# Kernel tuning notes

Measured on AMD Instinct MI355X. Metric: run time of the kernel, lower is better.

## Reference

```python
import jax, jax.numpy as jnp
import numpy as np

B, N, DM, S = 128, 1024, 64, 2
D_IN = 1 + 1 + 2 + DM  # x(1) + m(1) + u(2) + h(DM)


def setup_inputs() -> dict:
    key = jax.random.key(0)
    ks = jax.random.split(key, 12)
    return {
        "x": jax.random.normal(ks[0], (B, 1, N), jnp.float32),
        "m": jax.random.uniform(ks[1], (B, 1, N), jnp.float32),
        "u": jax.random.normal(ks[2], (B, 2, N), jnp.float32),
        "h": jax.random.normal(ks[3], (B, DM, N), jnp.float32),
        # stack of support_len row-normalized-ish adjacencies [S, N, N]
        "adj": jax.random.uniform(ks[4], (S, N, N), jnp.float32) / N,
        "W_in": jax.random.normal(ks[5], (DM, D_IN), jnp.float32) * 0.05,
        "b_in": jnp.zeros((DM,), jnp.float32),
        "W_gc": jax.random.normal(ks[6], (DM, S * DM), jnp.float32) * 0.05,
        "b_gc": jnp.zeros((DM,), jnp.float32),
        "W_out": jax.random.normal(ks[7], (DM, 2 * DM), jnp.float32) * 0.05,
        "b_out": jnp.zeros((DM,), jnp.float32),
        "W_read": jax.random.normal(ks[8], (1, 2 * DM), jnp.float32) * 0.05,
        "b_read": jnp.zeros((1,), jnp.float32),
        "prelu_w": jnp.full((1,), 0.25, jnp.float32),
    }


def _conv1x1(x, W, b):
    # Conv1d(kernel_size=1): [b,c,n] x [o,c] -> [b,o,n]
    return jnp.einsum('bcn,oc->bon', x, W) + b[None, :, None]


def reference(x, m, u, h, adj, W_in, b_in, W_gc, b_gc, W_out, b_out, W_read, b_read, prelu_w):
    # concat inputs on channel dim, then 1x1 conv to d_model
    x_in = jnp.concatenate([x, m, u, h], axis=1)            # [b, d_in, n]
    x_in = _conv1x1(x_in, W_in, b_in)                        # [b, dm, n]
    # SpatialConvOrderK (order=1, include_self=False):
    # per-support aggregation einsum('ncvl,wv->ncwl') with l==1
    agg = jnp.einsum('bcv,swv->bscw', x_in, adj)             # [b, S, dm, n]
    b_, s_, c_, n_ = agg.shape
    agg = agg.reshape(b_, s_ * c_, n_)                       # support-major concat
    gc = _conv1x1(agg, W_gc, b_gc)                           # [b, dm, n]
    out = jnp.concatenate([gc, h], axis=1)                   # [b, 2dm, n]
    out = _conv1x1(out, W_out, b_out)
    out = jnp.where(out >= 0, out, prelu_w[0] * out)         # PReLU (1 param)
    out = jnp.concatenate([out, h], axis=1)                  # [b, 2dm, n]
    return _conv1x1(out, W_read, b_read), out
```

## Files before the change

kernel.cpp:

```cpp
#include <hip/hip_runtime.h>
#include <hip/hip_bf16.h>
#include <stdint.h>

#define NB 128
#define NN 1024
#define NDM 64

typedef __bf16 bf16;
typedef __bf16 bf16x8_t __attribute__((ext_vector_type(8)));
typedef __bf16 bf16x4_t __attribute__((ext_vector_type(4)));
typedef float f32x4 __attribute__((ext_vector_type(4)));

__global__ __launch_bounds__(256) void k_prep(
    const float* __restrict__ adj,
    const float* __restrict__ W_in, const float* __restrict__ b_in,
    const float* __restrict__ W_gc, const float* __restrict__ b_gc,
    const float* __restrict__ W_out, const float* __restrict__ b_out,
    const float* __restrict__ W_read,
    bf16* __restrict__ adjb, bf16* __restrict__ WAT, float* __restrict__ WYX,
    float* __restrict__ BIAS, bf16* __restrict__ W1B, bf16* __restrict__ A2B,
    float* __restrict__ HBv) {
  const int bx = blockIdx.x;
  if (bx < 2048) {
    int i = bx * 256 + threadIdx.x;
    float4 v = reinterpret_cast<const float4*>(adj)[i];
    bf16x4_t r;
    r.x = (bf16)v.x; r.y = (bf16)v.y; r.z = (bf16)v.z; r.w = (bf16)v.w;
    reinterpret_cast<bf16x4_t*>(adjb)[i] = r;
    return;
  }
  int i = (bx - 2048) * 256 + threadIdx.x;
  if (i < 8192) {
    int r = i >> 6, cc = i & 63;
    int cq = cc >> 3, j = cc & 7;
    int c = ((cq ^ (r & 7)) << 3) + j;
    int s = r >> 6, o = r & 63;
    float val = 0.f;
    for (int k = 0; k < 64; ++k) val += W_gc[o * 128 + s * 64 + k] * W_in[k * 68 + 4 + c];
    WAT[i] = (bf16)val;
  } else if (i < 8704) {
    int idx = i - 8192;
    int r = idx >> 2, jj = idx & 3;
    int s = r >> 6, o = r & 63;
    float val = 0.f;
    for (int k = 0; k < 64; ++k) val += W_gc[o * 128 + s * 64 + k] * W_in[k * 68 + jj];
    WYX[idx] = val;
  } else if (i < 8832) {
    int r = i - 8704;
    int s = r >> 6, o = r & 63;
    float val = 0.f;
    for (int k = 0; k < 64; ++k) val += W_gc[o * 128 + s * 64 + k] * b_in[k];
    BIAS[r] = val;
  } else if (i < 12928) {
    int j = i - 8832;
    int o = j >> 6, c = j & 63;
    W1B[j] = (bf16)W_out[o * 128 + c];
  } else if (i < 18048) {
    int j = i - 12928;
    int r = j >> 6, c = j & 63;
    float val = 0.f;
    if (r < 64) val = W_out[r * 128 + 64 + c];
    else if (r == 64) val = W_read[64 + c];
    A2B[j] = (bf16)val;
  } else if (i < 18112) {
    int o = i - 18048;
    float val = b_out[o];
    for (int c = 0; c < 64; ++c) val += W_out[o * 128 + c] * b_gc[c];
    HBv[o] = val;
  }
}

__global__ __launch_bounds__(256) void k_build(
    const float* __restrict__ x, const float* __restrict__ m, const float* __restrict__ u,
    const float* __restrict__ h, const bf16* __restrict__ WAT,
    const float* __restrict__ WYX, const float* __restrict__ BIAS,
    bf16* __restrict__ Y, bf16* __restrict__ HT, float* __restrict__ out2) {
  __shared__ __align__(16) float T[64 * 128];
  __shared__ __align__(16) bf16 HTs[128 * 64];
  __shared__ __align__(16) bf16 WAs[128 * 64];
  __shared__ __align__(16) float X4L[128 * 4];
  __shared__ __align__(16) float WYXs[128 * 4];
  __shared__ __align__(16) float biasL[128];
  const int t = threadIdx.x;
  const int vb = blockIdx.x * 128;
  const int b = blockIdx.y;

  for (int i = t; i < 2048; i += 256)
    __builtin_amdgcn_global_load_lds(
        (const uint32_t*)(h + (size_t)(b * 64 + (i >> 5)) * NN + vb + (i & 31) * 4),
        (uint32_t*)&T[i * 4], 16, 0, 0);
  for (int i = t; i < 1024; i += 256)
    __builtin_amdgcn_global_load_lds((const uint32_t*)(WAT + i * 8), (uint32_t*)&WAs[i * 8], 16, 0, 0);
  if (t < 128)
    __builtin_amdgcn_global_load_lds((const uint32_t*)(WYX + t * 4), (uint32_t*)&WYXs[t * 4], 16, 0, 0);
  if (t < 32)
    __builtin_amdgcn_global_load_lds((const uint32_t*)(BIAS + t * 4), (uint32_t*)&biasL[t * 4], 16, 0, 0);
  if (t < 128) {
    float4 x4;
    x4.x = x[(size_t)b * NN + vb + t];
    x4.y = m[(size_t)b * NN + vb + t];
    x4.z = u[(size_t)(b * 2) * NN + vb + t];
    x4.w = u[(size_t)(b * 2 + 1) * NN + vb + t];
    *reinterpret_cast<float4*>(&X4L[t * 4]) = x4;
  }
  __syncthreads();

  {
    const int v = t >> 1, half = t & 1;
#pragma unroll
    for (int cc = 0; cc < 4; ++cc) {
      int cq = half * 4 + cc;
      int cbase = (cq ^ (v & 7)) << 3;
      bf16x8_t pk;
#pragma unroll
      for (int j = 0; j < 8; ++j) pk[j] = (bf16)T[(cbase + j) * 128 + v];
      *reinterpret_cast<bf16x8_t*>(&HTs[v * 64 + cq * 8]) = pk;
      *reinterpret_cast<bf16x8_t*>(&HT[((size_t)(b << 10) + vb + v) * 64 + cq * 8]) = pk;
    }
  }
  for (int i = t; i < 2048; i += 256) {
    int r = i >> 5, ck = i & 31;
    float4 hv = *reinterpret_cast<const float4*>(&T[r * 128 + ck * 4]);
    *reinterpret_cast<float4*>(&out2[(size_t)(b * 128 + 64 + r) * NN + vb + ck * 4]) = hv;
  }
  __syncthreads();

  const int wave = t >> 6, lane = t & 63;
  const int q = lane >> 4, lx = lane & 7, o16 = lane & 15;
  const int offK0 = (q ^ lx) << 3, offK1 = ((q + 4) ^ lx) << 3;

#pragma unroll
  for (int vi = 0; vi < 2; ++vi) {
    const int vt = wave + vi * 4;
    const int vrow = vt * 16 + o16;
    bf16x8_t af0 = *reinterpret_cast<const bf16x8_t*>(&HTs[vrow * 64 + offK0]);
    bf16x8_t af1 = *reinterpret_cast<const bf16x8_t*>(&HTs[vrow * 64 + offK1]);
    float4 x4r[4];
#pragma unroll
    for (int r = 0; r < 4; ++r)
      x4r[r] = *reinterpret_cast<const float4*>(&X4L[(vt * 16 + q * 4 + r) * 4]);
    const int vg = vb + vt * 16 + q * 4;
    for (int nt = 0; nt < 8; ++nt) {
      const int rr = nt * 16 + o16;
      bf16x8_t bf0 = *reinterpret_cast<const bf16x8_t*>(&WAs[rr * 64 + offK0]);
      bf16x8_t bf1 = *reinterpret_cast<const bf16x8_t*>(&WAs[rr * 64 + offK1]);
      float bsv = biasL[rr];
      float4 wy = *reinterpret_cast<const float4*>(&WYXs[rr * 4]);
      f32x4 c0;
#pragma unroll
      for (int r = 0; r < 4; ++r)
        c0[r] = bsv + wy.x * x4r[r].x + wy.y * x4r[r].y + wy.z * x4r[r].z + wy.w * x4r[r].w;
      f32x4 acc = __builtin_amdgcn_mfma_f32_16x16x32_bf16(af0, bf0, c0, 0, 0, 0);
      acc = __builtin_amdgcn_mfma_f32_16x16x32_bf16(af1, bf1, acc, 0, 0, 0);
      const int s = nt >> 2;
      const int o = rr - s * 64;
      bf16x4_t pk;
      pk.x = (bf16)acc[0]; pk.y = (bf16)acc[1]; pk.z = (bf16)acc[2]; pk.w = (bf16)acc[3];
      *reinterpret_cast<bf16x4_t*>(&Y[(size_t)(b * 64 + o) * 2048 + s * 1024 + vg]) = pk;
    }
  }
}

__global__ __launch_bounds__(256) void k_gemm(
    const bf16* __restrict__ Y, const bf16* __restrict__ ADJB,
    const bf16* __restrict__ HT,
    const bf16* __restrict__ W1B, const bf16* __restrict__ A2B,
    const float* __restrict__ HBv, const float* __restrict__ W_read,
    const float* __restrict__ b_read, const float* __restrict__ prelu_w,
    float* __restrict__ out0, float* __restrict__ out2) {
  __shared__ __align__(16) union SMem {
    struct { bf16 As[128 * 64]; bf16 Bs[128 * 64]; } st;
    bf16 gcs[2 * 128 * 72];
  } sm;
  __shared__ __align__(16) bf16 W1s[64 * 72];
  __shared__ __align__(16) bf16 A2s[80 * 72];
  __shared__ float HBs[64];
  __shared__ float Wrs[64];

  const int t = threadIdx.x;
  const int wave = t >> 6, lane = t & 63;
  const int rowA = blockIdx.x * 128;
  const int colB = blockIdx.y * 128;
  const int wm = (wave & 1) * 64, wn = (wave >> 1) * 64;
  const int fr = lane & 15;
  const int q = lane >> 4, lx = lane & 7;
  const int offK0 = (q ^ lx) << 3, offK1 = ((q + 4) ^ lx) << 3;

  for (int i = t; i < 4096; i += 256) W1s[(i >> 6) * 72 + (i & 63)] = W1B[i];
  for (int i = t; i < 5120; i += 256) A2s[(i >> 6) * 72 + (i & 63)] = A2B[i];
  if (t < 64) { HBs[t] = HBv[t]; Wrs[t] = W_read[t]; }
  const float pw = prelu_w[0];
  const float br = b_read[0];

  f32x4 acc[4][4];
  const f32x4 zero = {0.f, 0.f, 0.f, 0.f};
#pragma unroll
  for (int i = 0; i < 4; ++i)
#pragma unroll
    for (int j = 0; j < 4; ++j) acc[i][j] = zero;

  const bf16* aSrc[4]; const bf16* bSrc[4];
  uint32_t* aDst[4]; uint32_t* bDst[4];
#pragma unroll
  for (int j = 0; j < 4; ++j) {
    int c = t + 256 * j;
    int row = c >> 3;
    int qs = (c & 7) ^ (row & 7);
    aSrc[j] = Y + (size_t)(rowA + row) * 2048 + qs * 8;
    bSrc[j] = ADJB + (size_t)(colB + row) * 1024 + qs * 8;
    aDst[j] = (uint32_t*)&sm.st.As[c * 8];
    bDst[j] = (uint32_t*)&sm.st.Bs[c * 8];
  }
  int rAb[4], rBb[4];
#pragma unroll
  for (int i = 0; i < 4; ++i) {
    rAb[i] = (wm + i * 16 + fr) * 64;
    rBb[i] = (wn + i * 16 + fr) * 64;
  }
  __syncthreads();

  for (int s = 0; s < 2; ++s) {
    for (int kk = 0; kk < 1024; kk += 64) {
#pragma unroll
      for (int j = 0; j < 4; ++j) {
        __builtin_amdgcn_global_load_lds((const uint32_t*)aSrc[j], aDst[j], 16, 0, 0);
        aSrc[j] += 64;
      }
#pragma unroll
      for (int j = 0; j < 4; ++j) {
        __builtin_amdgcn_global_load_lds((const uint32_t*)bSrc[j], bDst[j], 16, 0, 0);
        bSrc[j] += 64;
      }
      __syncthreads();
#pragma unroll
      for (int k2 = 0; k2 < 2; ++k2) {
        const int off = k2 ? offK1 : offK0;
        bf16x8_t af[4], bfr[4];
#pragma unroll
        for (int i = 0; i < 4; ++i)
          af[i] = *reinterpret_cast<const bf16x8_t*>(&sm.st.As[rAb[i] + off]);
#pragma unroll
        for (int i = 0; i < 4; ++i)
          bfr[i] = *reinterpret_cast<const bf16x8_t*>(&sm.st.Bs[rBb[i] + off]);
#pragma unroll
        for (int i = 0; i < 4; ++i)
#pragma unroll
          for (int j = 0; j < 4; ++j)
            acc[i][j] = __builtin_amdgcn_mfma_f32_16x16x32_bf16(af[i], bfr[j], acc[i][j], 0, 0, 0);
      }
      __syncthreads();
    }
    if (s == 0) {
#pragma unroll
      for (int j = 0; j < 4; ++j) bSrc[j] += (1024 * 1024 - 1024);
    }
  }

  {
    const int b2w = wm >> 6;
#pragma unroll
    for (int i = 0; i < 4; ++i) {
      const int cc0 = i * 16 + q * 4;
#pragma unroll
      for (int j = 0; j < 4; ++j) {
        const int wl = wn + j * 16 + fr;
        bf16x4_t r;
        r.x = (bf16)acc[i][j][0]; r.y = (bf16)acc[i][j][1];
        r.z = (bf16)acc[i][j][2]; r.w = (bf16)acc[i][j][3];
        *reinterpret_cast<bf16x4_t*>(&sm.gcs[b2w * 9216 + wl * 72 + cc0]) = r;
      }
    }
  }
  __syncthreads();

  const int b2 = wave >> 1, jh = wave & 1;
  const int b = blockIdx.x * 2 + b2;

  f32x4 acc2[5][4];
#pragma unroll
  for (int i = 0; i < 5; ++i)
#pragma unroll
    for (int j = 0; j < 4; ++j) {
      if (i < 4) {
        f32x4 c0;
#pragma unroll
        for (int r = 0; r < 4; ++r) c0[r] = HBs[i * 16 + q * 4 + r];
        acc2[i][j] = c0;
      } else {
        acc2[i][j] = zero;
      }
    }

#pragma unroll
  for (int k2 = 0; k2 < 64; k2 += 32) {
    bf16x8_t af2[4], bf2[4];
#pragma unroll
    for (int i = 0; i < 4; ++i)
      af2[i] = *reinterpret_cast<const bf16x8_t*>(&W1s[(i * 16 + fr) * 72 + k2 + q * 8]);
#pragma unroll
    for (int j = 0; j < 4; ++j)
      bf2[j] = *reinterpret_cast<const bf16x8_t*>(&sm.gcs[b2 * 9216 + (jh * 64 + j * 16 + fr) * 72 + k2 + q * 8]);
#pragma unroll
    for (int i = 0; i < 4; ++i)
#pragma unroll
      for (int j = 0; j < 4; ++j)
        acc2[i][j] = __builtin_amdgcn_mfma_f32_16x16x32_bf16(af2[i], bf2[j], acc2[i][j], 0, 0, 0);
  }

#pragma unroll
  for (int k2 = 0; k2 < 64; k2 += 32) {
    const int off = k2 ? offK1 : offK0;
    bf16x8_t bh[4], af3[5];
#pragma unroll
    for (int j = 0; j < 4; ++j) {
      const int w = colB + jh * 64 + j * 16 + fr;
      bh[j] = *reinterpret_cast<const bf16x8_t*>(&HT[((size_t)(b << 10) + w) * 64 + off]);
    }
#pragma unroll
    for (int i = 0; i < 5; ++i)
      af3[i] = *reinterpret_cast<const bf16x8_t*>(&A2s[(i * 16 + fr) * 72 + k2 + q * 8]);
#pragma unroll
    for (int i = 0; i < 5; ++i)
#pragma unroll
      for (int j = 0; j < 4; ++j)
        acc2[i][j] = __builtin_amdgcn_mfma_f32_16x16x32_bf16(af3[i], bh[j], acc2[i][j], 0, 0, 0);
  }

  float rd[4] = {0.f, 0.f, 0.f, 0.f};
#pragma unroll
  for (int i = 0; i < 4; ++i) {
#pragma unroll
    for (int r = 0; r < 4; ++r) {
      const int o = i * 16 + q * 4 + r;
      const float wr = Wrs[o];
#pragma unroll
      for (int j = 0; j < 4; ++j) {
        const int wg = colB + jh * 64 + j * 16 + fr;
        float val = acc2[i][j][r];
        val = val >= 0.f ? val : pw * val;
        out2[(size_t)(b * 128 + o) * 1024 + wg] = val;
        rd[j] += wr * val;
      }
    }
  }
#pragma unroll
  for (int j = 0; j < 4; ++j) {
    rd[j] += __shfl_xor(rd[j], 16, 64);
    rd[j] += __shfl_xor(rd[j], 32, 64);
  }
  if (lane < 16) {
#pragma unroll
    for (int j = 0; j < 4; ++j) {
      const int wg = colB + jh * 64 + j * 16 + lane;
      out0[(size_t)b * 1024 + wg] = rd[j] + acc2[4][j][0] + br;
    }
  }
}

extern "C" void kernel_launch(void* const* d_in, const int* in_sizes, int n_in,
                              void* d_out, int out_size, void* d_ws, size_t ws_size,
                              hipStream_t stream) {
  (void)in_sizes; (void)n_in; (void)out_size; (void)ws_size;
  const float* x       = (const float*)d_in[0];
  const float* m       = (const float*)d_in[1];
  const float* u       = (const float*)d_in[2];
  const float* h       = (const float*)d_in[3];
  const float* adj     = (const float*)d_in[4];
  const float* W_in    = (const float*)d_in[5];
  const float* b_in    = (const float*)d_in[6];
  const float* W_gc    = (const float*)d_in[7];
  const float* b_gc    = (const float*)d_in[8];
  const float* W_out   = (const float*)d_in[9];
  const float* b_out   = (const float*)d_in[10];
  const float* W_read  = (const float*)d_in[11];
  const float* b_read  = (const float*)d_in[12];
  const float* prelu_w = (const float*)d_in[13];

  char* ws = (char*)d_ws;
  bf16*  Y    = (bf16*)(ws);
  bf16*  ADJB = (bf16*)(ws + 33554432);
  bf16*  HT   = (bf16*)(ws + 37748736);
  bf16*  WAT  = (bf16*)(ws + 54525952);
  float* WYX  = (float*)(ws + 54542336);
  float* BIAS = (float*)(ws + 54544384);
  bf16*  W1B  = (bf16*)(ws + 54544896);
  bf16*  A2B  = (bf16*)(ws + 54553088);
  float* HBv  = (float*)(ws + 54563328);

  float* out0 = (float*)d_out;
  float* out2 = out0 + 131072;

  hipLaunchKernelGGL(k_prep,  dim3(2119),     dim3(256), 0, stream,
                     adj, W_in, b_in, W_gc, b_gc, W_out, b_out, W_read,
                     ADJB, WAT, WYX, BIAS, W1B, A2B, HBv);
  hipLaunchKernelGGL(k_build, dim3(8, 128),   dim3(256), 0, stream,
                     x, m, u, h, WAT, WYX, BIAS, Y, HT, out2);
  hipLaunchKernelGGL(k_gemm,  dim3(64, 8),    dim3(256), 0, stream,
                     Y, ADJB, HT, W1B, A2B, HBv, W_read, b_read, prelu_w, out0, out2);
}
```

Before: 183.9 us.

## Shrink k_gemm tile to one batch per block, raising occupancy

The main adjacency GEMM block now covers one batch (64 rows) by 128 columns instead of two batches. Each wave owns a 64x32 sub-tile, and the launch bounds ask for 4 blocks per CU. The W1/A2 weight staging in shared memory is dropped and those fragments are read straight from global memory. The intent is smaller LDS and register footprint, so more blocks fit per CU and the grid doubles to 1024 blocks. In exchange, each block reloads the ADJB B-tile per batch, so B traffic doubles and operand reuse per MFMA drops.

```diff
diff --git a/kernel.cpp b/kernel.cpp
--- a/kernel.cpp
+++ b/kernel.cpp
@@ -161,7 +161,7 @@
   }
 }
 
-__global__ __launch_bounds__(256) void k_gemm(
+__global__ __launch_bounds__(256, 4) void k_gemm(
     const bf16* __restrict__ Y, const bf16* __restrict__ ADJB,
     const bf16* __restrict__ HT,
     const bf16* __restrict__ W1B, const bf16* __restrict__ A2B,
@@ -169,60 +169,61 @@
     const float* __restrict__ b_read, const float* __restrict__ prelu_w,
     float* __restrict__ out0, float* __restrict__ out2) {
   __shared__ __align__(16) union SMem {
-    struct { bf16 As[128 * 64]; bf16 Bs[128 * 64]; } st;
-    bf16 gcs[2 * 128 * 72];
+    struct { bf16 As[64 * 64]; bf16 Bs[128 * 64]; } st;
+    bf16 gcs[128 * 72];
   } sm;
-  __shared__ __align__(16) bf16 W1s[64 * 72];
-  __shared__ __align__(16) bf16 A2s[80 * 72];
   __shared__ float HBs[64];
   __shared__ float Wrs[64];
 
   const int t = threadIdx.x;
   const int wave = t >> 6, lane = t & 63;
-  const int rowA = blockIdx.x * 128;
+  const int b = blockIdx.x;
   const int colB = blockIdx.y * 128;
-  const int wm = (wave & 1) * 64, wn = (wave >> 1) * 64;
   const int fr = lane & 15;
   const int q = lane >> 4, lx = lane & 7;
   const int offK0 = (q ^ lx) << 3, offK1 = ((q + 4) ^ lx) << 3;
-
-  for (int i = t; i < 4096; i += 256) W1s[(i >> 6) * 72 + (i & 63)] = W1B[i];
-  for (int i = t; i < 5120; i += 256) A2s[(i >> 6) * 72 + (i & 63)] = A2B[i];
+  const int wn = wave * 32;
+
   if (t < 64) { HBs[t] = HBv[t]; Wrs[t] = W_read[t]; }
   const float pw = prelu_w[0];
   const float br = b_read[0];
 
-  f32x4 acc[4][4];
+  f32x4 acc[4][2];
   const f32x4 zero = {0.f, 0.f, 0.f, 0.f};
 #pragma unroll
   for (int i = 0; i < 4; ++i)
 #pragma unroll
-    for (int j = 0; j < 4; ++j) acc[i][j] = zero;
-
-  const bf16* aSrc[4]; const bf16* bSrc[4];
-  uint32_t* aDst[4]; uint32_t* bDst[4];
+    for (int j = 0; j < 2; ++j) acc[i][j] = zero;
+
+  const bf16* aSrc[2]; uint32_t* aDst[2];
+#pragma unroll
+  for (int j = 0; j < 2; ++j) {
+    int c = t + 256 * j;
+    int row = c >> 3;
+    int qs = (c & 7) ^ (row & 7);
+    aSrc[j] = Y + (size_t)(b * 64 + row) * 2048 + qs * 8;
+    aDst[j] = (uint32_t*)&sm.st.As[c * 8];
+  }
+  const bf16* bSrc[4]; uint32_t* bDst[4];
 #pragma unroll
   for (int j = 0; j < 4; ++j) {
     int c = t + 256 * j;
     int row = c >> 3;
     int qs = (c & 7) ^ (row & 7);
-    aSrc[j] = Y + (size_t)(rowA + row) * 2048 + qs * 8;
     bSrc[j] = ADJB + (size_t)(colB + row) * 1024 + qs * 8;
-    aDst[j] = (uint32_t*)&sm.st.As[c * 8];
     bDst[j] = (uint32_t*)&sm.st.Bs[c * 8];
   }
-  int rAb[4], rBb[4];
-#pragma unroll
-  for (int i = 0; i < 4; ++i) {
-    rAb[i] = (wm + i * 16 + fr) * 64;
-    rBb[i] = (wn + i * 16 + fr) * 64;
-  }
+  int rAb[4], rBb[2];
+#pragma unroll
+  for (int i = 0; i < 4; ++i) rAb[i] = (i * 16 + fr) * 64;
+#pragma unroll
+  for (int j = 0; j < 2; ++j) rBb[j] = (wn + j * 16 + fr) * 64;
   __syncthreads();
 
   for (int s = 0; s < 2; ++s) {
     for (int kk = 0; kk < 1024; kk += 64) {
 #pragma unroll
-      for (int j = 0; j < 4; ++j) {
+      for (int j = 0; j < 2; ++j) {
         __builtin_amdgcn_global_load_lds((const uint32_t*)aSrc[j], aDst[j], 16, 0, 0);
         aSrc[j] += 64;
       }
@@ -235,17 +236,17 @@
 #pragma unroll
       for (int k2 = 0; k2 < 2; ++k2) {
         const int off = k2 ? offK1 : offK0;
-        bf16x8_t af[4], bfr[4];
+        bf16x8_t af[4], bfr[2];
 #pragma unroll
         for (int i = 0; i < 4; ++i)
           af[i] = *reinterpret_cast<const bf16x8_t*>(&sm.st.As[rAb[i] + off]);
 #pragma unroll
+        for (int j = 0; j < 2; ++j)
+          bfr[j] = *reinterpret_cast<const bf16x8_t*>(&sm.st.Bs[rBb[j] + off]);
+#pragma unroll
         for (int i = 0; i < 4; ++i)
-          bfr[i] = *reinterpret_cast<const bf16x8_t*>(&sm.st.Bs[rBb[i] + off]);
-#pragma unroll
-        for (int i = 0; i < 4; ++i)
-#pragma unroll
-          for (int j = 0; j < 4; ++j)
+#pragma unroll
+          for (int j = 0; j < 2; ++j)
             acc[i][j] = __builtin_amdgcn_mfma_f32_16x16x32_bf16(af[i], bfr[j], acc[i][j], 0, 0, 0);
       }
       __syncthreads();
@@ -256,31 +257,25 @@
     }
   }
 
-  {
-    const int b2w = wm >> 6;
-#pragma unroll
-    for (int i = 0; i < 4; ++i) {
-      const int cc0 = i * 16 + q * 4;
-#pragma unroll
-      for (int j = 0; j < 4; ++j) {
-        const int wl = wn + j * 16 + fr;
-        bf16x4_t r;
-        r.x = (bf16)acc[i][j][0]; r.y = (bf16)acc[i][j][1];
-        r.z = (bf16)acc[i][j][2]; r.w = (bf16)acc[i][j][3];
-        *reinterpret_cast<bf16x4_t*>(&sm.gcs[b2w * 9216 + wl * 72 + cc0]) = r;
-      }
+#pragma unroll
+  for (int i = 0; i < 4; ++i) {
+    const int cc0 = i * 16 + q * 4;
+#pragma unroll
+    for (int j = 0; j < 2; ++j) {
+      const int wl = wn + j * 16 + fr;
+      bf16x4_t r;
+      r.x = (bf16)acc[i][j][0]; r.y = (bf16)acc[i][j][1];
+      r.z = (bf16)acc[i][j][2]; r.w = (bf16)acc[i][j][3];
+      *reinterpret_cast<bf16x4_t*>(&sm.gcs[wl * 72 + cc0]) = r;
     }
   }
   __syncthreads();
 
-  const int b2 = wave >> 1, jh = wave & 1;
-  const int b = blockIdx.x * 2 + b2;
-
-  f32x4 acc2[5][4];
+  f32x4 acc2[5][2];
 #pragma unroll
   for (int i = 0; i < 5; ++i)
 #pragma unroll
-    for (int j = 0; j < 4; ++j) {
+    for (int j = 0; j < 2; ++j) {
       if (i < 4) {
         f32x4 c0;
 #pragma unroll
@@ -292,41 +287,38 @@
     }
 
 #pragma unroll
-  for (int k2 = 0; k2 < 64; k2 += 32) {
-    bf16x8_t af2[4], bf2[4];
+  for (int k2i = 0; k2i < 2; ++k2i) {
+    const int k2 = k2i * 32;
+    const int off = k2i ? offK1 : offK0;
+    bf16x8_t af2[4], bf2[2];
 #pragma unroll
     for (int i = 0; i < 4; ++i)
-      af2[i] = *reinterpret_cast<const bf16x8_t*>(&W1s[(i * 16 + fr) * 72 + k2 + q * 8]);
-#pragma unroll
-    for (int j = 0; j < 4; ++j)
-      bf2[j] = *reinterpret_cast<const bf16x8_t*>(&sm.gcs[b2 * 9216 + (jh * 64 + j * 16 + fr) * 72 + k2 + q * 8]);
+      af2[i] = *reinterpret_cast<const bf16x8_t*>(&W1B[(i * 16 + fr) * 64 + k2 + q * 8]);
+#pragma unroll
+    for (int j = 0; j < 2; ++j)
+      bf2[j] = *reinterpret_cast<const bf16x8_t*>(&sm.gcs[(wn + j * 16 + fr) * 72 + k2 + q * 8]);
 #pragma unroll
     for (int i = 0; i < 4; ++i)
 #pragma unroll
-      for (int j = 0; j < 4; ++j)
+      for (int j = 0; j < 2; ++j)
         acc2[i][j] = __builtin_amdgcn_mfma_f32_16x16x32_bf16(af2[i], bf2[j], acc2[i][j], 0, 0, 0);
-  }
-
-#pragma unroll
-  for (int k2 = 0; k2 < 64; k2 += 32) {
-    const int off = k2 ? offK1 : offK0;
-    bf16x8_t bh[4], af3[5];
-#pragma unroll
-    for (int j = 0; j < 4; ++j) {
-      const int w = colB + jh * 64 + j * 16 + fr;
+    bf16x8_t af3[5], bh[2];
+#pragma unroll
+    for (int i = 0; i < 5; ++i)
+      af3[i] = *reinterpret_cast<const bf16x8_t*>(&A2B[(i * 16 + fr) * 64 + k2 + q * 8]);
+#pragma unroll
+    for (int j = 0; j < 2; ++j) {
+      const int w = colB + wn + j * 16 + fr;
       bh[j] = *reinterpret_cast<const bf16x8_t*>(&HT[((size_t)(b << 10) + w) * 64 + off]);
     }
 #pragma unroll
     for (int i = 0; i < 5; ++i)
-      af3[i] = *reinterpret_cast<const bf16x8_t*>(&A2s[(i * 16 + fr) * 72 + k2 + q * 8]);
-#pragma unroll
-    for (int i = 0; i < 5; ++i)
-#pragma unroll
-      for (int j = 0; j < 4; ++j)
+#pragma unroll
+      for (int j = 0; j < 2; ++j)
         acc2[i][j] = __builtin_amdgcn_mfma_f32_16x16x32_bf16(af3[i], bh[j], acc2[i][j], 0, 0, 0);
   }
 
-  float rd[4] = {0.f, 0.f, 0.f, 0.f};
+  float rd[2] = {0.f, 0.f};
 #pragma unroll
   for (int i = 0; i < 4; ++i) {
 #pragma unroll
@@ -334,8 +326,8 @@
       const int o = i * 16 + q * 4 + r;
       const float wr = Wrs[o];
 #pragma unroll
-      for (int j = 0; j < 4; ++j) {
-        const int wg = colB + jh * 64 + j * 16 + fr;
+      for (int j = 0; j < 2; ++j) {
+        const int wg = colB + wn + j * 16 + fr;
         float val = acc2[i][j][r];
         val = val >= 0.f ? val : pw * val;
         out2[(size_t)(b * 128 + o) * 1024 + wg] = val;
@@ -344,14 +336,14 @@
     }
   }
 #pragma unroll
-  for (int j = 0; j < 4; ++j) {
+  for (int j = 0; j < 2; ++j) {
     rd[j] += __shfl_xor(rd[j], 16, 64);
     rd[j] += __shfl_xor(rd[j], 32, 64);
   }
   if (lane < 16) {
 #pragma unroll
-    for (int j = 0; j < 4; ++j) {
-      const int wg = colB + jh * 64 + j * 16 + lane;
+    for (int j = 0; j < 2; ++j) {
+      const int wg = colB + wn + j * 16 + lane;
       out0[(size_t)b * 1024 + wg] = rd[j] + acc2[4][j][0] + br;
     }
   }
@@ -395,6 +387,6 @@
                      ADJB, WAT, WYX, BIAS, W1B, A2B, HBv);
   hipLaunchKernelGGL(k_build, dim3(8, 128),   dim3(256), 0, stream,
                      x, m, u, h, WAT, WYX, BIAS, Y, HT, out2);
-  hipLaunchKernelGGL(k_gemm,  dim3(64, 8),    dim3(256), 0, stream,
+  hipLaunchKernelGGL(k_gemm,  dim3(128, 8),   dim3(256), 0, stream,
                      Y, ADJB, HT, W1B, A2B, HBv, W_read, b_read, prelu_w, out0, out2);
 }
```

After: 189.5 us. 3.1% more time.
